# Kernel optimization log

Hardware: AMD Instinct MI355X
Metric: run time of the kernel (lower is better)

## Reference

```python
import jax, jax.numpy as jnp
import numpy as np
from jax import lax

B, T, H, V = 4, 2048, 512, 32000


def setup_inputs() -> dict:
    key = jax.random.key(0)
    ks = jax.random.split(key, 8)
    s = 0.05
    return {
        'input': jax.random.randint(ks[0], (B, T), 0, V),
        'h0': jnp.zeros((1, B, H), jnp.float32),
        'c0': jnp.zeros((1, B, H), jnp.float32),
        'emb': jax.random.uniform(ks[1], (V, H), jnp.float32, -0.1, 0.1),
        'W_ih': jax.random.normal(ks[2], (4 * H, H), jnp.float32) * s,
        'W_hh': jax.random.normal(ks[3], (4 * H, H), jnp.float32) * s,
        'b_ih': jnp.zeros((4 * H,), jnp.float32),
        'b_hh': jnp.zeros((4 * H,), jnp.float32),
        'Wa1': jax.random.normal(ks[4], (H, H), jnp.float32) * s,
        'ba1': jnp.zeros((H,), jnp.float32),
        'wa2': jax.random.normal(ks[5], (1, H), jnp.float32) * s,
        'ba2': jnp.zeros((1,), jnp.float32),
        'Wc': jax.random.normal(ks[6], (H, 2 * H), jnp.float32) * s,
        'bc': jnp.zeros((H,), jnp.float32),
        'b_dec': jnp.zeros((V,), jnp.float32),
    }


def _lstm(x, h0, c0, W_ih, W_hh, b_ih, b_hh):
    # x: [B,T,E]; PyTorch gate order i,f,g,o
    xg = jnp.einsum('bte,ge->btg', x, W_ih) + b_ih + b_hh  # [B,T,4H]

    def step(carry, xt):
        h, c = carry
        g = xt + h @ W_hh.T
        i, f, gg, o = jnp.split(g, 4, axis=-1)
        c = jax.nn.sigmoid(f) * c + jax.nn.sigmoid(i) * jnp.tanh(gg)
        h = jax.nn.sigmoid(o) * jnp.tanh(c)
        return (h, c), h

    (_, _), hs = lax.scan(step, (h0, c0), xg.transpose(1, 0, 2))
    return hs.transpose(1, 0, 2)  # [B,T,H]


def reference(input, h0, c0, emb, W_ih, W_hh, b_ih, b_hh, Wa1, ba1, wa2, ba2, Wc, bc, b_dec):
    x = emb[input]                                   # [B,T,H] embedding lookup
    enc = _lstm(x, h0[0], c0[0], W_ih, W_hh, b_ih, b_hh)  # [B,T,H]
    # attention scores (scalar per timestep, query-independent)
    s = (jnp.tanh(enc @ Wa1.T + ba1) @ wa2.T + ba2)[..., 0]  # [B,T]
    # causal softmax pooling via O(T) prefix sums (softmax is shift-invariant)
    e = jnp.exp(s - jnp.max(s, axis=1, keepdims=True))       # [B,T]
    num = jnp.cumsum(e[..., None] * enc, axis=1)             # [B,T,H]
    den = jnp.cumsum(e, axis=1)[..., None]                   # [B,T,1]
    ctx = num / den                                          # [B,T,H]
    combined = jnp.tanh(jnp.concatenate([ctx, enc], axis=-1) @ Wc.T + bc)
    decoded = combined @ emb.T + b_dec                       # tied decoder [B,T,V]
    return decoded
```

## Files before the change

### kernel.cpp

```cpp
#include <hip/hip_runtime.h>

#define BB 4
#define TT 2048
#define HH 512
#define GH 2048
#define VV 32000
#define MM 8192
#define LBLK 64

typedef unsigned short u16;
typedef short bfrag8 __attribute__((ext_vector_type(8)));
typedef float f32x4  __attribute__((ext_vector_type(4)));

static __device__ __forceinline__ u16 f2bf(float f) {
    unsigned x = __float_as_uint(f);
    unsigned r = x + 0x7fffu + ((x >> 16) & 1u);
    return (u16)(r >> 16);
}
static __device__ __forceinline__ float bf2f(u16 u) {
    return __uint_as_float(((unsigned)u) << 16);
}
static __device__ __forceinline__ float sigm(float x) {
    return 1.0f / (1.0f + __expf(-x));
}
static __device__ __forceinline__ float tanh_f(float x) {
    x = fminf(fmaxf(x, -30.f), 30.f);
    float e = __expf(2.f * x);
    return (e - 1.f) / (e + 1.f);
}


__global__ void k_zero(int* __restrict__ p, int n) {
    int i = blockIdx.x * 256 + threadIdx.x;
    if (i < n) p[i] = 0;
}

__global__ void k_cast_bf16(const float* __restrict__ in, u16* __restrict__ out, int n4) {
    int i = blockIdx.x * 256 + threadIdx.x;
    if (i < n4) {
        float4 v = ((const float4*)in)[i];
        ushort4 o;
        o.x = f2bf(v.x); o.y = f2bf(v.y); o.z = f2bf(v.z); o.w = f2bf(v.w);
        ((ushort4*)out)[i] = o;
    }
}

__global__ void k_bias_sum(const float* __restrict__ a, const float* __restrict__ b,
                           float* __restrict__ o) {
    int i = blockIdx.x * 256 + threadIdx.x;
    if (i < GH) o[i] = a[i] + b[i];
}

__global__ void k_gather(const u16* __restrict__ embb, const int* __restrict__ ids,
                         u16* __restrict__ xb) {
    int m = blockIdx.x * 2 + (threadIdx.x >> 7);
    int l = threadIdx.x & 127;
    int id = ids[m];
    ((uint2*)(xb + (size_t)m * HH))[l] = ((const uint2*)(embb + (size_t)id * HH))[l];
}

__global__ __launch_bounds__(256) void k_gemm_nt(
    const u16* __restrict__ A, const u16* __restrict__ Bm,
    float* __restrict__ Cf, u16* __restrict__ Cb,
    const float* __restrict__ bias, int M, int N, int K, int dotanh)
{
    __shared__ u16 As[128][32];
    __shared__ u16 Bs[128][32];
    const int tid  = threadIdx.x;
    const int lane = tid & 63, wid = tid >> 6;
    const int wm = (wid >> 1) * 64, wn = (wid & 1) * 64;
    const int lr = lane & 15, lq = lane >> 4;
    const int m0 = blockIdx.y * 128, n0 = blockIdx.x * 128;
    const int srow = tid >> 1, skh = (tid & 1) * 16;

    f32x4 acc[4][4];
    for (int i = 0; i < 4; ++i)
        for (int j = 0; j < 4; ++j) { f32x4 z = {0.f, 0.f, 0.f, 0.f}; acc[i][j] = z; }

    const u16* ag = A  + (size_t)(m0 + srow) * K + skh;
    const u16* bg = Bm + (size_t)(n0 + srow) * K + skh;

    for (int k0 = 0; k0 < K; k0 += 32) {
        uint4 av0 = *(const uint4*)(ag + k0);
        uint4 av1 = *(const uint4*)(ag + k0 + 8);
        uint4 bv0 = *(const uint4*)(bg + k0);
        uint4 bv1 = *(const uint4*)(bg + k0 + 8);
        __syncthreads();
        *(uint4*)&As[srow][skh]     = av0;
        *(uint4*)&As[srow][skh + 8] = av1;
        *(uint4*)&Bs[srow][skh]     = bv0;
        *(uint4*)&Bs[srow][skh + 8] = bv1;
        __syncthreads();
        bfrag8 af[4], bf[4];
#pragma unroll
        for (int mt = 0; mt < 4; ++mt) af[mt] = *(const bfrag8*)&As[wm + mt * 16 + lr][lq * 8];
#pragma unroll
        for (int nt = 0; nt < 4; ++nt) bf[nt] = *(const bfrag8*)&Bs[wn + nt * 16 + lr][lq * 8];
#pragma unroll
        for (int mt = 0; mt < 4; ++mt)
#pragma unroll
            for (int nt = 0; nt < 4; ++nt)
                acc[mt][nt] = __builtin_amdgcn_mfma_f32_16x16x32_bf16(af[mt], bf[nt], acc[mt][nt], 0, 0, 0);
    }

#pragma unroll
    for (int mt = 0; mt < 4; ++mt)
#pragma unroll
        for (int nt = 0; nt < 4; ++nt) {
            int col = n0 + wn + nt * 16 + lr;
            float bv = bias ? bias[col] : 0.f;
#pragma unroll
            for (int r = 0; r < 4; ++r) {
                int row = m0 + wm + mt * 16 + lq * 4 + r;
                float v = acc[mt][nt][r] + bv;
                if (dotanh) v = tanhf(v);
                size_t off = (size_t)row * N + col;
                if (Cf) Cf[off] = v;
                if (Cb) Cb[off] = f2bf(v);
            }
        }
}

__global__ __launch_bounds__(256) void k_lstm(
    const float* __restrict__ Whh, const float* __restrict__ xg,
    const float* __restrict__ h0, const float* __restrict__ c0,
    float* __restrict__ enc, u16* __restrict__ encb,
    int* __restrict__ flags)
{
    const int tid = threadIdx.x, blk = blockIdx.x;
    const int rq = tid & 7;
    const int seg = tid >> 3;
    __shared__ float hbuf[4][512];
    __shared__ float red[4][4][8][36];
    __shared__ float gsum[4][4][8];
    __shared__ float cl[4][8];

    float4 w4[4][4];
#pragma unroll
    for (int g = 0; g < 4; ++g)
#pragma unroll
        for (int q = 0; q < 4; ++q)
            w4[g][q] = *(const float4*)&Whh[(size_t)(g * HH + blk * 8 + rq) * HH + seg * 16 + q * 4];

    if (tid < 32) { int b = tid >> 3, d = tid & 7; cl[b][d] = c0[b * HH + blk * 8 + d]; }

    const int e0 = tid * 8, hb = e0 >> 9, hk = e0 & 511;

    for (int t = 0; t < TT; ++t) {
        float xv = 0.f;
        if (tid < 128) {
            int pd = tid & 7, pg = (tid >> 3) & 3, pb = tid >> 5;
            xv = xg[(size_t)(pb * TT + t) * GH + pg * HH + blk * 8 + pd];
        }
        if (t == 0) {
            *(float4*)&hbuf[hb][hk]     = *(const float4*)&h0[hb * HH + hk];
            *(float4*)&hbuf[hb][hk + 4] = *(const float4*)&h0[hb * HH + hk + 4];
        } else {
            if (tid < 64) {
                while (__hip_atomic_load(&flags[(t - 1) * LBLK + tid],
                                         __ATOMIC_RELAXED, __HIP_MEMORY_SCOPE_AGENT) == 0) {}
            }
            __syncthreads();
            const float* src = &enc[(size_t)(hb * TT + (t - 1)) * HH + hk];
            float v[8];
#pragma unroll
            for (int j = 0; j < 8; ++j)
                v[j] = __hip_atomic_load(src + j, __ATOMIC_RELAXED, __HIP_MEMORY_SCOPE_AGENT);
#pragma unroll
            for (int j = 0; j < 8; ++j) hbuf[hb][hk + j] = v[j];
        }
        __syncthreads();

        float acc[4][4] = {};
#pragma unroll
        for (int q = 0; q < 4; ++q) {
            float4 h4[4];
#pragma unroll
            for (int b = 0; b < 4; ++b) h4[b] = *(const float4*)&hbuf[b][seg * 16 + q * 4];
#pragma unroll
            for (int g = 0; g < 4; ++g)
#pragma unroll
                for (int b = 0; b < 4; ++b) {
                    acc[g][b] = fmaf(w4[g][q].x, h4[b].x, acc[g][b]);
                    acc[g][b] = fmaf(w4[g][q].y, h4[b].y, acc[g][b]);
                    acc[g][b] = fmaf(w4[g][q].z, h4[b].z, acc[g][b]);
                    acc[g][b] = fmaf(w4[g][q].w, h4[b].w, acc[g][b]);
                }
        }
#pragma unroll
        for (int g = 0; g < 4; ++g)
#pragma unroll
            for (int b = 0; b < 4; ++b) red[g][b][rq][seg] = acc[g][b];
        __syncthreads();

        if (tid < 128) {
            int d = tid & 7, g = (tid >> 3) & 3, b = tid >> 5;
            const float4* rp = (const float4*)red[g][b][d];
            float4 s4 = rp[0];
#pragma unroll
            for (int j = 1; j < 8; ++j) {
                float4 v = rp[j];
                s4.x += v.x; s4.y += v.y; s4.z += v.z; s4.w += v.w;
            }
            gsum[g][b][d] = (s4.x + s4.y) + (s4.z + s4.w) + xv;
        }
        __syncthreads();

        if (tid < 64) {
            if (tid < 32) {
                int b = tid >> 3, d = tid & 7;
                float gi = gsum[0][b][d], gf = gsum[1][b][d], gg = gsum[2][b][d], go = gsum[3][b][d];
                float c  = cl[b][d];
                float cn = sigm(gf) * c + sigm(gi) * tanh_f(gg);
                float hn = sigm(go) * tanh_f(cn);
                cl[b][d] = cn;
                size_t oi = (size_t)(b * TT + t) * HH + blk * 8 + d;
                __hip_atomic_store(&enc[oi], hn, __ATOMIC_RELAXED, __HIP_MEMORY_SCOPE_AGENT);
                encb[oi] = f2bf(hn);
            }
            asm volatile("s_waitcnt vmcnt(0)" ::: "memory");
            if (tid == 0)
                __hip_atomic_store(&flags[t * LBLK + blk], 1,
                                   __ATOMIC_RELAXED, __HIP_MEMORY_SCOPE_AGENT);
        }
    }
}

__global__ __launch_bounds__(256) void k_scores(const float* __restrict__ tb,
        const float* __restrict__ wa2, const float* __restrict__ ba2, float* __restrict__ sb)
{
    int m = blockIdx.x * 4 + (threadIdx.x >> 6);
    int lane = threadIdx.x & 63;
    const float4* p = (const float4*)(tb + (size_t)m * HH + lane * 8);
    const float4* w = (const float4*)(wa2 + lane * 8);
    float4 v0 = p[0], v1 = p[1], w0 = w[0], w1 = w[1];
    float r = v0.x * w0.x + v0.y * w0.y + v0.z * w0.z + v0.w * w0.w
            + v1.x * w1.x + v1.y * w1.y + v1.z * w1.z + v1.w * w1.w;
    for (int off = 32; off; off >>= 1) r += __shfl_down(r, off);
    if (lane == 0) sb[m] = r + ba2[0];
}

__global__ __launch_bounds__(256) void k_softd(const float* __restrict__ s,
        float* __restrict__ e, float* __restrict__ invden)
{
    __shared__ float lred[256];
    __shared__ float pref[256];
    int tid = threadIdx.x;
    for (int b = 0; b < BB; ++b) {
        const float* sb = s + b * TT;
        float m = -1e30f;
#pragma unroll
        for (int j = 0; j < 8; ++j) m = fmaxf(m, sb[tid * 8 + j]);
        lred[tid] = m;
        __syncthreads();
        for (int off = 128; off; off >>= 1) {
            if (tid < off) lred[tid] = fmaxf(lred[tid], lred[tid + off]);
            __syncthreads();
        }
        float mx = lred[0];
        __syncthreads();
        float es[8]; float cs = 0.f;
#pragma unroll
        for (int j = 0; j < 8; ++j) { es[j] = expf(sb[tid * 8 + j] - mx); cs += es[j]; }
        pref[tid] = cs;
        __syncthreads();
        if (tid == 0) {
            float run = 0.f;
            for (int i = 0; i < 256; ++i) { float v = pref[i]; pref[i] = run; run += v; }
        }
        __syncthreads();
        float run = pref[tid];
#pragma unroll
        for (int j = 0; j < 8; ++j) {
            run += es[j];
            e[b * TT + tid * 8 + j] = es[j];
            invden[b * TT + tid * 8 + j] = 1.0f / run;
        }
        __syncthreads();
    }
}

__global__ __launch_bounds__(256) void k_ctx(const u16* __restrict__ encb,
        const float* __restrict__ e, const float* __restrict__ invden, u16* __restrict__ cat)
{
    int g = blockIdx.x * 256 + threadIdx.x;
    int b = g >> 9, h = g & 511;
    float acc = 0.f;
    for (int t = 0; t < TT; ++t) {
        size_t m = (size_t)b * TT + t;
        u16 hu = encb[m * HH + h];
        acc = fmaf(e[m], bf2f(hu), acc);
        float ctx = acc * invden[m];
        cat[m * 1024 + h]       = f2bf(ctx);
        cat[m * 1024 + 512 + h] = hu;
    }
}

extern "C" void kernel_launch(void* const* d_in, const int* in_sizes, int n_in,
                              void* d_out, int out_size, void* d_ws, size_t ws_size,
                              hipStream_t stream)
{
    const int*   ids   = (const int*)  d_in[0];
    const float* h0    = (const float*)d_in[1];
    const float* c0    = (const float*)d_in[2];
    const float* emb   = (const float*)d_in[3];
    const float* W_ih  = (const float*)d_in[4];
    const float* W_hh  = (const float*)d_in[5];
    const float* b_ih  = (const float*)d_in[6];
    const float* b_hh  = (const float*)d_in[7];
    const float* Wa1   = (const float*)d_in[8];
    const float* ba1   = (const float*)d_in[9];
    const float* wa2   = (const float*)d_in[10];
    const float* ba2   = (const float*)d_in[11];
    const float* Wc    = (const float*)d_in[12];
    const float* bc    = (const float*)d_in[13];
    const float* b_dec = (const float*)d_in[14];
    float* out = (float*)d_out;

    char* w = (char*)d_ws;
    auto carve = [&](size_t bytes) { char* p = w; w += (bytes + 255) & ~(size_t)255; return p; };
    int*  flags  = (int*) carve((size_t)LBLK * TT * 4);
    u16*  embb   = (u16*) carve((size_t)VV * HH * 2);
    u16*  wihb   = (u16*) carve((size_t)GH * HH * 2);
    u16*  wa1b   = (u16*) carve((size_t)HH * HH * 2);
    u16*  wcb    = (u16*) carve((size_t)HH * 1024 * 2);
    float* bsum  = (float*)carve((size_t)GH * 4);
    u16*  xb     = (u16*) carve((size_t)MM * HH * 2);
    float* xg    = (float*)carve((size_t)MM * GH * 4);
    float* enc   = (float*)carve((size_t)MM * HH * 4);
    u16*  encb   = (u16*) carve((size_t)MM * HH * 2);
    float* tanhb = (float*)carve((size_t)MM * HH * 4);
    float* sbuf  = (float*)carve((size_t)MM * 4);
    float* ebuf  = (float*)carve((size_t)MM * 4);
    float* invd  = (float*)carve((size_t)MM * 4);
    u16*  catb   = (u16*) carve((size_t)MM * 1024 * 2);
    u16*  combb  = (u16*) carve((size_t)MM * HH * 2);

    k_zero<<<dim3(512), dim3(256), 0, stream>>>(flags, LBLK * TT);
    k_cast_bf16<<<dim3(VV * HH / 4 / 256), dim3(256), 0, stream>>>(emb, embb, VV * HH / 4);
    k_cast_bf16<<<dim3(GH * HH / 4 / 256), dim3(256), 0, stream>>>(W_ih, wihb, GH * HH / 4);
    k_cast_bf16<<<dim3(HH * HH / 4 / 256), dim3(256), 0, stream>>>(Wa1, wa1b, HH * HH / 4);
    k_cast_bf16<<<dim3(HH * 1024 / 4 / 256), dim3(256), 0, stream>>>(Wc, wcb, HH * 1024 / 4);
    k_bias_sum<<<dim3(8), dim3(256), 0, stream>>>(b_ih, b_hh, bsum);
    k_gather<<<dim3(MM / 2), dim3(256), 0, stream>>>(embb, ids, xb);

    k_gemm_nt<<<dim3(GH / 128, MM / 128), dim3(256), 0, stream>>>(
        xb, wihb, xg, nullptr, bsum, MM, GH, HH, 0);

    k_lstm<<<dim3(LBLK), dim3(256), 0, stream>>>(W_hh, xg, h0, c0, enc, encb, flags);

    k_gemm_nt<<<dim3(HH / 128, MM / 128), dim3(256), 0, stream>>>(
        encb, wa1b, tanhb, nullptr, ba1, MM, HH, HH, 1);

    k_scores<<<dim3(MM / 4), dim3(256), 0, stream>>>(tanhb, wa2, ba2, sbuf);
    k_softd<<<dim3(1), dim3(256), 0, stream>>>(sbuf, ebuf, invd);
    k_ctx<<<dim3(8), dim3(256), 0, stream>>>(encb, ebuf, invd, catb);

    k_gemm_nt<<<dim3(HH / 128, MM / 128), dim3(256), 0, stream>>>(
        catb, wcb, nullptr, combb, bc, MM, HH, 1024, 1);

    k_gemm_nt<<<dim3(VV / 128, MM / 128), dim3(256), 0, stream>>>(
        combb, embb, out, nullptr, b_dec, MM, VV, HH, 0);
}
```

Measured before the change: 11.22 ms.

## Replace per-step flag handshake in LSTM with canary-value polling on data

The persistent LSTM kernel no longer publishes per-block ready flags after each timestep. Consumers instead spin directly on the hidden-state values, which are pre-filled with a NaN canary pattern, until all eight loaded words differ from it. This removes one flag store, a vmcnt wait, a flag spin and a block barrier from the serial critical path of each step. In exchange the whole enc buffer must be filled before launch, and correctness depends on the canary never being a real output and on each word becoming visible whole.

```diff
diff --git a/kernel.cpp b/kernel.cpp
--- a/kernel.cpp
+++ b/kernel.cpp
@@ -7,6 +7,7 @@
 #define VV 32000
 #define MM 8192
 #define LBLK 64
+#define CANARY 0x7F800001u
 
 typedef unsigned short u16;
 typedef short bfrag8 __attribute__((ext_vector_type(8)));
@@ -30,9 +31,12 @@
 }
 
 
-__global__ void k_zero(int* __restrict__ p, int n) {
+__global__ void k_fill(unsigned* __restrict__ p, unsigned v, int n4) {
     int i = blockIdx.x * 256 + threadIdx.x;
-    if (i < n) p[i] = 0;
+    if (i < n4) {
+        uint4 q = {v, v, v, v};
+        ((uint4*)p)[i] = q;
+    }
 }
 
 __global__ void k_cast_bf16(const float* __restrict__ in, u16* __restrict__ out, int n4) {
@@ -124,8 +128,7 @@
 __global__ __launch_bounds__(256) void k_lstm(
     const float* __restrict__ Whh, const float* __restrict__ xg,
     const float* __restrict__ h0, const float* __restrict__ c0,
-    float* __restrict__ enc, u16* __restrict__ encb,
-    int* __restrict__ flags)
+    float* __restrict__ enc, u16* __restrict__ encb)
 {
     const int tid = threadIdx.x, blk = blockIdx.x;
     const int rq = tid & 7;
@@ -156,18 +159,20 @@
             *(float4*)&hbuf[hb][hk]     = *(const float4*)&h0[hb * HH + hk];
             *(float4*)&hbuf[hb][hk + 4] = *(const float4*)&h0[hb * HH + hk + 4];
         } else {
-            if (tid < 64) {
-                while (__hip_atomic_load(&flags[(t - 1) * LBLK + tid],
-                                         __ATOMIC_RELAXED, __HIP_MEMORY_SCOPE_AGENT) == 0) {}
-            }
-            __syncthreads();
-            const float* src = &enc[(size_t)(hb * TT + (t - 1)) * HH + hk];
-            float v[8];
-#pragma unroll
-            for (int j = 0; j < 8; ++j)
-                v[j] = __hip_atomic_load(src + j, __ATOMIC_RELAXED, __HIP_MEMORY_SCOPE_AGENT);
-#pragma unroll
-            for (int j = 0; j < 8; ++j) hbuf[hb][hk + j] = v[j];
+            const int* srci = (const int*)&enc[(size_t)(hb * TT + (t - 1)) * HH + hk];
+            int v[8];
+            bool ok;
+            do {
+                ok = true;
+#pragma unroll
+                for (int j = 0; j < 8; ++j) {
+                    v[j] = __hip_atomic_load(srci + j, __ATOMIC_RELAXED,
+                                             __HIP_MEMORY_SCOPE_AGENT);
+                    ok = ok && ((unsigned)v[j] != CANARY);
+                }
+            } while (!ok);
+#pragma unroll
+            for (int j = 0; j < 8; ++j) hbuf[hb][hk + j] = __int_as_float(v[j]);
         }
         __syncthreads();
 
@@ -206,22 +211,16 @@
         }
         __syncthreads();
 
-        if (tid < 64) {
-            if (tid < 32) {
-                int b = tid >> 3, d = tid & 7;
-                float gi = gsum[0][b][d], gf = gsum[1][b][d], gg = gsum[2][b][d], go = gsum[3][b][d];
-                float c  = cl[b][d];
-                float cn = sigm(gf) * c + sigm(gi) * tanh_f(gg);
-                float hn = sigm(go) * tanh_f(cn);
-                cl[b][d] = cn;
-                size_t oi = (size_t)(b * TT + t) * HH + blk * 8 + d;
-                __hip_atomic_store(&enc[oi], hn, __ATOMIC_RELAXED, __HIP_MEMORY_SCOPE_AGENT);
-                encb[oi] = f2bf(hn);
-            }
-            asm volatile("s_waitcnt vmcnt(0)" ::: "memory");
-            if (tid == 0)
-                __hip_atomic_store(&flags[t * LBLK + blk], 1,
-                                   __ATOMIC_RELAXED, __HIP_MEMORY_SCOPE_AGENT);
+        if (tid < 32) {
+            int b = tid >> 3, d = tid & 7;
+            float gi = gsum[0][b][d], gf = gsum[1][b][d], gg = gsum[2][b][d], go = gsum[3][b][d];
+            float c  = cl[b][d];
+            float cn = sigm(gf) * c + sigm(gi) * tanh_f(gg);
+            float hn = sigm(go) * tanh_f(cn);
+            cl[b][d] = cn;
+            size_t oi = (size_t)(b * TT + t) * HH + blk * 8 + d;
+            __hip_atomic_store(&enc[oi], hn, __ATOMIC_RELAXED, __HIP_MEMORY_SCOPE_AGENT);
+            encb[oi] = f2bf(hn);
         }
     }
 }
@@ -319,7 +318,6 @@
 
     char* w = (char*)d_ws;
     auto carve = [&](size_t bytes) { char* p = w; w += (bytes + 255) & ~(size_t)255; return p; };
-    int*  flags  = (int*) carve((size_t)LBLK * TT * 4);
     u16*  embb   = (u16*) carve((size_t)VV * HH * 2);
     u16*  wihb   = (u16*) carve((size_t)GH * HH * 2);
     u16*  wa1b   = (u16*) carve((size_t)HH * HH * 2);
@@ -336,7 +334,8 @@
     u16*  catb   = (u16*) carve((size_t)MM * 1024 * 2);
     u16*  combb  = (u16*) carve((size_t)MM * HH * 2);
 
-    k_zero<<<dim3(512), dim3(256), 0, stream>>>(flags, LBLK * TT);
+    k_fill<<<dim3(MM * HH / 4 / 256), dim3(256), 0, stream>>>(
+        (unsigned*)enc, CANARY, MM * HH / 4);
     k_cast_bf16<<<dim3(VV * HH / 4 / 256), dim3(256), 0, stream>>>(emb, embb, VV * HH / 4);
     k_cast_bf16<<<dim3(GH * HH / 4 / 256), dim3(256), 0, stream>>>(W_ih, wihb, GH * HH / 4);
     k_cast_bf16<<<dim3(HH * HH / 4 / 256), dim3(256), 0, stream>>>(Wa1, wa1b, HH * HH / 4);
@@ -347,7 +346,7 @@
     k_gemm_nt<<<dim3(GH / 128, MM / 128), dim3(256), 0, stream>>>(
         xb, wihb, xg, nullptr, bsum, MM, GH, HH, 0);
 
-    k_lstm<<<dim3(LBLK), dim3(256), 0, stream>>>(W_hh, xg, h0, c0, enc, encb, flags);
+    k_lstm<<<dim3(LBLK), dim3(256), 0, stream>>>(W_hh, xg, h0, c0, enc, encb);
 
     k_gemm_nt<<<dim3(HH / 128, MM / 128), dim3(256), 0, stream>>>(
         encb, wa1b, tanhb, nullptr, ba1, MM, HH, HH, 1);
```

New measurement: 10.39 ms. -7.4%, faster.
